# Performance work log

Hardware: AMD Instinct MI355X
Metric: run time of the kernel (lower is better)

Reference implementation:

```python
import jax, jax.numpy as jnp
import numpy as np

N = 50000
E = 800000
IN = 128
H = 128
R = 8
OUT = 2
BN_EPS = 1e-5


def setup_inputs() -> dict:
    key = jax.random.key(0)
    ks = jax.random.split(key, 16)
    s1 = 1.0 / np.sqrt(IN)
    s2 = 1.0 / np.sqrt(H)
    return {
        "x": jax.random.normal(ks[0], (N, IN), dtype=jnp.float32),
        "edge_index": jax.random.randint(ks[1], (2, E), 0, N, dtype=jnp.int32),
        "edge_type": jax.random.randint(ks[2], (E,), 0, R, dtype=jnp.int32),
        # layer 1 RGCNConv params
        "w1": jax.random.normal(ks[3], (R, IN, H), dtype=jnp.float32) * s1,
        "root1": jax.random.normal(ks[4], (IN, H), dtype=jnp.float32) * s1,
        "b1": jnp.zeros((H,), dtype=jnp.float32),
        "g1": jnp.ones((H,), dtype=jnp.float32),
        "be1": jnp.zeros((H,), dtype=jnp.float32),
        # layer 2 RGCNConv params
        "w2": jax.random.normal(ks[5], (R, H, H), dtype=jnp.float32) * s2,
        "root2": jax.random.normal(ks[6], (H, H), dtype=jnp.float32) * s2,
        "b2": jnp.zeros((H,), dtype=jnp.float32),
        "g2": jnp.ones((H,), dtype=jnp.float32),
        "be2": jnp.zeros((H,), dtype=jnp.float32),
        # classifier
        "cw": jax.random.normal(ks[7], (H, OUT), dtype=jnp.float32) * s2,
        "cb": jnp.zeros((OUT,), dtype=jnp.float32),
    }


def rgcn_conv(x, src, tgt, et, W, root, b):
    """PyG-style RGCNConv with per-relation mean aggregation.

    out[v] = sum_r mean_{e: tgt=v, type=r} (x[src_e] @ W[r]) + x[v] @ root + b
    """
    n = x.shape[0]
    # per-(node, relation) in-degree for mean normalization
    comp = tgt * R + et  # composite segment id, [E]
    deg = jax.ops.segment_sum(jnp.ones_like(et, dtype=x.dtype), comp,
                              num_segments=n * R)
    inv_deg = jnp.where(deg > 0, 1.0 / jnp.maximum(deg, 1.0), 0.0)
    # transform every node by every relation weight: [n, R, out]
    xw = jnp.einsum('ni,rio->nro', x, W)
    # gather per-edge message and apply mean normalization: [E, out]
    msg = xw[src, et] * inv_deg[comp][:, None]
    agg = jax.ops.segment_sum(msg, tgt, num_segments=n)
    return agg + x @ root + b


def batchnorm(x, gamma, beta):
    # training-mode BatchNorm1d over node dim (biased variance, eps=1e-5)
    mean = jnp.mean(x, axis=0)
    var = jnp.mean(jnp.square(x - mean), axis=0)
    return gamma * (x - mean) * jax.lax.rsqrt(var + BN_EPS) + beta


def reference(x, edge_index, edge_type, w1, root1, b1, g1, be1,
              w2, root2, b2, g2, be2, cw, cb):
    src, tgt = edge_index[0], edge_index[1]
    h = rgcn_conv(x, src, tgt, edge_type, w1, root1, b1)
    h = jax.nn.relu(batchnorm(h, g1, be1))
    h = rgcn_conv(h, src, tgt, edge_type, w2, root2, b2)
    h = jax.nn.relu(batchnorm(h, g2, be2))
    return h @ cw + cb
```

## Files before the change

kernel.cpp:

```cpp
#include <hip/hip_runtime.h>
#include <hip/hip_bf16.h>

#define N_NODES 50000
#define N_EDGES 800000
#define DIM 128
#define NREL 8
#define KTOT 1152
#define NRSEG (N_NODES * NREL)
#define BN_EPS 1e-5f
#define TILE 32
#define ASTRIDE 136

typedef __attribute__((ext_vector_type(8))) short bf16x8;
typedef __attribute__((ext_vector_type(16))) float f32x16;

__device__ inline float b2f(short s) {
    union { unsigned u; float f; } t;
    t.u = ((unsigned)(unsigned short)s) << 16;
    return t.f;
}
__device__ inline short f2b(float f) {
    __hip_bfloat16 h = __float2bfloat16(f);
    return *reinterpret_cast<short*>(&h);
}


__global__ void k_hist(const int* __restrict__ ei, const int* __restrict__ et,
                       int* __restrict__ cnt) {
    int e = blockIdx.x * 256 + threadIdx.x;
    if (e < N_EDGES) {
        int tgt = ei[N_EDGES + e];
        int r = et[e];
        atomicAdd(&cnt[tgt * NREL + r], 1);
    }
}

__global__ void k_alloc(const int* __restrict__ cnt, int* __restrict__ offs,
                        int* __restrict__ cursor) {
    int i = blockIdx.x * 256 + threadIdx.x;
    int lane = threadIdx.x & 63;
    int c = (i < NRSEG) ? cnt[i] : 0;
    int incl = c;
    #pragma unroll
    for (int d = 1; d < 64; d <<= 1) {
        int t = __shfl_up(incl, d, 64);
        if (lane >= d) incl += t;
    }
    int total = __shfl(incl, 63, 64);
    int base = 0;
    if (lane == 63) base = atomicAdd(cursor, total);
    base = __shfl(base, 63, 64);
    if (i < NRSEG) offs[i] = base + incl - c;
}

__global__ void k_fill(const int* __restrict__ ei, const int* __restrict__ et,
                       const int* __restrict__ offs, int* __restrict__ fillcur,
                       int* __restrict__ sorted) {
    int e = blockIdx.x * 256 + threadIdx.x;
    if (e < N_EDGES) {
        int src = ei[e];
        int tgt = ei[N_EDGES + e];
        int comp = tgt * NREL + et[e];
        int pos = atomicAdd(&fillcur[comp], 1);
        sorted[offs[comp] + pos] = src;
    }
}

__global__ void k_wconv2(const float* __restrict__ W1, const float* __restrict__ root1,
                         __hip_bfloat16* __restrict__ Bt1,
                         const float* __restrict__ W2, const float* __restrict__ root2,
                         __hip_bfloat16* __restrict__ Bt2) {
    int gidx = blockIdx.x * 256 + threadIdx.x;
    int which = gidx >= DIM * KTOT;
    int idx = which ? gidx - DIM * KTOT : gidx;
    const float* W = which ? W2 : W1;
    const float* root = which ? root2 : root1;
    __hip_bfloat16* Bt = which ? Bt2 : Bt1;
    int o = idx / KTOT, k = idx % KTOT;
    float v;
    if (k < NREL * DIM) {
        int r = k >> 7, i = k & 127;
        v = W[(r * DIM + i) * DIM + o];
    } else {
        int i = k - NREL * DIM;
        v = root[i * DIM + o];
    }
    Bt[idx] = __float2bfloat16(v);
}

__global__ void k_cast(const float* __restrict__ in, __hip_bfloat16* __restrict__ out) {
    int i = (blockIdx.x * 256 + threadIdx.x) * 4;
    if (i >= N_NODES * DIM) return;
    float4 v = *(const float4*)&in[i];
    short4 o;
    o.x = f2b(v.x); o.y = f2b(v.y); o.z = f2b(v.z); o.w = f2b(v.w);
    *(short4*)&out[i] = o;
}

__global__ void k_castbn2(const __hip_bfloat16* __restrict__ h, const float* __restrict__ stats,
                          const float* __restrict__ g, const float* __restrict__ be,
                          __hip_bfloat16* __restrict__ xb) {
    int i = (blockIdx.x * 256 + threadIdx.x) * 8;
    if (i >= N_NODES * DIM) return;
    int ch = i & 127;
    bf16x8 v = *(const bf16x8*)&h[i];
    const float invn = 1.f / (float)N_NODES;
    bf16x8 o;
    #pragma unroll
    for (int j = 0; j < 8; ++j) {
        float m = stats[ch + j] * invn;
        float var = stats[128 + ch + j] * invn - m * m;
        float a = g[ch + j] * rsqrtf(var + BN_EPS);
        float b = be[ch + j] - m * a;
        o[j] = f2b(fmaxf(b2f(v[j]) * a + b, 0.f));
    }
    *(bf16x8*)&xb[i] = o;
}

__global__ __launch_bounds__(256) void k_fusedC(
        const __hip_bfloat16* __restrict__ xb,
        const int* __restrict__ cnt, const int* __restrict__ offs,
        const int* __restrict__ sorted,
        const __hip_bfloat16* __restrict__ Bt,
        const float* __restrict__ bias,
        __hip_bfloat16* __restrict__ h, float* __restrict__ stats) {
    __shared__ __hip_bfloat16 At[TILE * ASTRIDE];
    __shared__ int cntS[TILE][NREL];
    __shared__ int offS[TILE][NREL];
    int tid = threadIdx.x;
    int n0 = blockIdx.x * TILE;

    {
        int ni = tid >> 3, r = tid & 7;
        int node = n0 + ni;
        int c = 0, o = 0;
        if (node < N_NODES) {
            c = cnt[node * NREL + r];
            o = offs[node * NREL + r];
        }
        cntS[ni][r] = c;
        offS[ni][r] = o;
    }
    __syncthreads();

    int lane = tid & 63, wid = tid >> 6;
    int half = lane >> 5, l31 = lane & 31;
    const __hip_bfloat16* bBase = Bt + (size_t)(wid * 32 + l31) * KTOT + half * 8;
    f32x16 acc = {};

    int spn = tid >> 4;
    int sub = tid & 15;
    const __hip_bfloat16* xsub = xb + sub * 8;

    #pragma unroll 1
    for (int r = 0; r < 9; ++r) {
        #pragma unroll
        for (int p = 0; p < 2; ++p) {
            int ni = p * 16 + spn;
            if (r < 8) {
                int c = cntS[ni][r];
                int o = offS[ni][r];
                float s[8] = {0.f,0.f,0.f,0.f,0.f,0.f,0.f,0.f};
                for (int i = 0; i < c; ++i) {
                    int idx = sorted[o + i];
                    bf16x8 rv = *(const bf16x8*)(xsub + (size_t)idx * DIM);
                    #pragma unroll
                    for (int j = 0; j < 8; ++j) s[j] += b2f(rv[j]);
                }
                float inv = (c > 0) ? 1.f / (float)c : 0.f;
                bf16x8 ov;
                #pragma unroll
                for (int j = 0; j < 8; ++j) ov[j] = f2b(s[j] * inv);
                *(bf16x8*)&At[ni * ASTRIDE + sub * 8] = ov;
            } else {
                int node = n0 + ni;
                bf16x8 sv = {};
                if (node < N_NODES) sv = *(const bf16x8*)(xsub + (size_t)node * DIM);
                *(bf16x8*)&At[ni * ASTRIDE + sub * 8] = sv;
            }
        }
        __syncthreads();
        const __hip_bfloat16* bs = bBase + r * DIM;
        #pragma unroll
        for (int m = 0; m < 8; ++m) {
            bf16x8 a = *(const bf16x8*)&At[l31 * ASTRIDE + m * 16 + half * 8];
            bf16x8 b = *(const bf16x8*)(bs + m * 16);
            acc = __builtin_amdgcn_mfma_f32_32x32x16_bf16(a, b, acc, 0, 0, 0);
        }
        __syncthreads();
    }

    int col = wid * 32 + l31;
    float bv = bias[col];
    float s1 = 0.f, s2 = 0.f;
    #pragma unroll
    for (int reg = 0; reg < 16; ++reg) {
        int row = n0 + (reg & 3) + 8 * (reg >> 2) + 4 * half;
        float v = acc[reg] + bv;
        if (row < N_NODES) {
            h[(size_t)row * DIM + col] = __float2bfloat16(v);
            s1 += v; s2 += v * v;
        }
    }
    s1 += __shfl_xor(s1, 32, 64);
    s2 += __shfl_xor(s2, 32, 64);
    if (half == 0) {
        atomicAdd(&stats[col], s1);
        atomicAdd(&stats[128 + col], s2);
    }
}

__global__ void k_classifier(const __hip_bfloat16* __restrict__ h, const float* __restrict__ stats,
                             const float* __restrict__ g, const float* __restrict__ be,
                             const float* __restrict__ cw, const float* __restrict__ cb,
                             float* __restrict__ out) {
    int w = blockIdx.x * 4 + (threadIdx.x >> 6);
    int lane = threadIdx.x & 63;
    if (w >= N_NODES) return;
    int c = lane * 2;
    const float invn = 1.f / (float)N_NODES;
    __hip_bfloat162 hv = *(const __hip_bfloat162*)&h[(size_t)w * DIM + c];
    float m0 = stats[c] * invn, var0 = stats[128 + c] * invn - m0 * m0;
    float a0 = g[c] * rsqrtf(var0 + BN_EPS), b0 = be[c] - m0 * a0;
    float m1 = stats[c + 1] * invn, var1 = stats[128 + c + 1] * invn - m1 * m1;
    float a1 = g[c + 1] * rsqrtf(var1 + BN_EPS), b1 = be[c + 1] - m1 * a1;
    float p0 = fmaxf(__bfloat162float(hv.x) * a0 + b0, 0.f);
    float p1 = fmaxf(__bfloat162float(hv.y) * a1 + b1, 0.f);
    float acc0 = p0 * cw[c * 2] + p1 * cw[(c + 1) * 2];
    float acc1 = p0 * cw[c * 2 + 1] + p1 * cw[(c + 1) * 2 + 1];
    #pragma unroll
    for (int d = 32; d; d >>= 1) {
        acc0 += __shfl_down(acc0, d, 64);
        acc1 += __shfl_down(acc1, d, 64);
    }
    if (lane == 0) {
        out[w * 2] = acc0 + cb[0];
        out[w * 2 + 1] = acc1 + cb[1];
    }
}

extern "C" void kernel_launch(void* const* d_in, const int* in_sizes, int n_in,
                              void* d_out, int out_size, void* d_ws, size_t ws_size,
                              hipStream_t stream) {
    const float* x    = (const float*)d_in[0];
    const int*   ei   = (const int*)d_in[1];
    const int*   et   = (const int*)d_in[2];
    const float* w1   = (const float*)d_in[3];
    const float* root1= (const float*)d_in[4];
    const float* b1   = (const float*)d_in[5];
    const float* g1   = (const float*)d_in[6];
    const float* be1  = (const float*)d_in[7];
    const float* w2   = (const float*)d_in[8];
    const float* root2= (const float*)d_in[9];
    const float* b2   = (const float*)d_in[10];
    const float* g2   = (const float*)d_in[11];
    const float* be2  = (const float*)d_in[12];
    const float* cw   = (const float*)d_in[13];
    const float* cb   = (const float*)d_in[14];
    float* out = (float*)d_out;

    char* ws = (char*)d_ws;
    size_t off = 0;
    auto alloc = [&](size_t bytes) -> char* {
        char* p = ws + off;
        off += (bytes + 255) & ~(size_t)255;
        return p;
    };
    int*   cnt     = (int*)alloc((size_t)NRSEG * 4);
    int*   fillcur = (int*)alloc((size_t)NRSEG * 4);
    int*   cursor  = (int*)alloc(256);
    float* stats1  = (float*)alloc(1024);
    float* stats2  = (float*)alloc(1024);
    size_t zero_bytes = off;
    int*   offs    = (int*)alloc((size_t)NRSEG * 4);
    __hip_bfloat16* Bt1 = (__hip_bfloat16*)alloc((size_t)DIM * KTOT * 2);
    __hip_bfloat16* Bt2 = (__hip_bfloat16*)alloc((size_t)DIM * KTOT * 2);
    int*   sorted  = (int*)alloc((size_t)N_EDGES * 4);
    __hip_bfloat16* xb = (__hip_bfloat16*)alloc((size_t)N_NODES * DIM * 2);
    __hip_bfloat16* h1 = (__hip_bfloat16*)alloc((size_t)N_NODES * DIM * 2);
    __hip_bfloat16* h2 = (__hip_bfloat16*)alloc((size_t)N_NODES * DIM * 2);

    hipMemsetAsync(d_ws, 0, zero_bytes, stream);

    k_hist<<<(N_EDGES + 255) / 256, 256, 0, stream>>>(ei, et, cnt);
    k_alloc<<<(NRSEG + 255) / 256, 256, 0, stream>>>(cnt, offs, cursor);
    k_fill<<<(N_EDGES + 255) / 256, 256, 0, stream>>>(ei, et, offs, fillcur, sorted);
    k_wconv2<<<2 * DIM * KTOT / 256, 256, 0, stream>>>(w1, root1, Bt1, w2, root2, Bt2);

    int fgrid = (N_NODES + TILE - 1) / TILE;

    k_cast<<<(N_NODES * DIM / 4 + 255) / 256, 256, 0, stream>>>(x, xb);
    k_fusedC<<<fgrid, 256, 0, stream>>>(xb, cnt, offs, sorted, Bt1, b1, h1, stats1);

    k_castbn2<<<(N_NODES * DIM / 8 + 255) / 256, 256, 0, stream>>>(h1, stats1, g1, be1, xb);
    k_fusedC<<<fgrid, 256, 0, stream>>>(xb, cnt, offs, sorted, Bt2, b2, h2, stats2);

    k_classifier<<<(N_NODES + 3) / 4, 256, 0, stream>>>(h2, stats2, g2, be2, cw, cb, out);
}
```

Baseline: 518.5 us.

## Fuse BN+ReLU into layer-2 gather and interleave two-node unrolled gathers

Removes the separate batchnorm/cast kernel. Layer 2 now reads h1 directly and applies the BN affine transform and ReLU on the fly to every gathered neighbour row and to the root row. The gather loop is also restructured to process two nodes at once, two edges per iteration, with masked loads, so more memory requests are in flight per thread. In exchange, the per-element BN math is recomputed for every edge rather than once per node. The sorted buffer gets padding so the reads past the end of a segment stay in bounds.

```diff
diff --git a/kernel.cpp b/kernel.cpp
--- a/kernel.cpp
+++ b/kernel.cpp
@@ -97,32 +97,15 @@
     *(short4*)&out[i] = o;
 }
 
-__global__ void k_castbn2(const __hip_bfloat16* __restrict__ h, const float* __restrict__ stats,
-                          const float* __restrict__ g, const float* __restrict__ be,
-                          __hip_bfloat16* __restrict__ xb) {
-    int i = (blockIdx.x * 256 + threadIdx.x) * 8;
-    if (i >= N_NODES * DIM) return;
-    int ch = i & 127;
-    bf16x8 v = *(const bf16x8*)&h[i];
-    const float invn = 1.f / (float)N_NODES;
-    bf16x8 o;
-    #pragma unroll
-    for (int j = 0; j < 8; ++j) {
-        float m = stats[ch + j] * invn;
-        float var = stats[128 + ch + j] * invn - m * m;
-        float a = g[ch + j] * rsqrtf(var + BN_EPS);
-        float b = be[ch + j] - m * a;
-        o[j] = f2b(fmaxf(b2f(v[j]) * a + b, 0.f));
-    }
-    *(bf16x8*)&xb[i] = o;
-}
-
-__global__ __launch_bounds__(256) void k_fusedC(
+template<int BN>
+__global__ __launch_bounds__(256) void k_fusedD(
         const __hip_bfloat16* __restrict__ xb,
         const int* __restrict__ cnt, const int* __restrict__ offs,
         const int* __restrict__ sorted,
         const __hip_bfloat16* __restrict__ Bt,
         const float* __restrict__ bias,
+        const float* __restrict__ bnstats, const float* __restrict__ g,
+        const float* __restrict__ be,
         __hip_bfloat16* __restrict__ h, float* __restrict__ stats) {
     __shared__ __hip_bfloat16 At[TILE * ASTRIDE];
     __shared__ int cntS[TILE][NREL];
@@ -141,41 +124,92 @@
         cntS[ni][r] = c;
         offS[ni][r] = o;
     }
-    __syncthreads();
 
     int lane = tid & 63, wid = tid >> 6;
     int half = lane >> 5, l31 = lane & 31;
     const __hip_bfloat16* bBase = Bt + (size_t)(wid * 32 + l31) * KTOT + half * 8;
     f32x16 acc = {};
 
-    int spn = tid >> 4;
-    int sub = tid & 15;
+    int spn = tid >> 4, sub = tid & 15;
     const __hip_bfloat16* xsub = xb + sub * 8;
+
+    float aC[8], bC[8];
+    if (BN) {
+        const float invn = 1.f / (float)N_NODES;
+        #pragma unroll
+        for (int j = 0; j < 8; ++j) {
+            int ch = sub * 8 + j;
+            float m = bnstats[ch] * invn;
+            float var = bnstats[128 + ch] * invn - m * m;
+            float aa = g[ch] * rsqrtf(var + BN_EPS);
+            aC[j] = aa;
+            bC[j] = be[ch] - m * aa;
+        }
+    }
+    __syncthreads();
 
     #pragma unroll 1
     for (int r = 0; r < 9; ++r) {
-        #pragma unroll
-        for (int p = 0; p < 2; ++p) {
-            int ni = p * 16 + spn;
-            if (r < 8) {
-                int c = cntS[ni][r];
-                int o = offS[ni][r];
-                float s[8] = {0.f,0.f,0.f,0.f,0.f,0.f,0.f,0.f};
-                for (int i = 0; i < c; ++i) {
-                    int idx = sorted[o + i];
-                    bf16x8 rv = *(const bf16x8*)(xsub + (size_t)idx * DIM);
-                    #pragma unroll
-                    for (int j = 0; j < 8; ++j) s[j] += b2f(rv[j]);
+        if (r < 8) {
+            int cA = cntS[spn][r],      oA = offS[spn][r];
+            int cB = cntS[spn + 16][r], oB = offS[spn + 16][r];
+            float sA[8] = {0.f,0.f,0.f,0.f,0.f,0.f,0.f,0.f};
+            float sB[8] = {0.f,0.f,0.f,0.f,0.f,0.f,0.f,0.f};
+            int mx = max(cA, cB);
+            #pragma unroll 1
+            for (int i = 0; i < mx; i += 2) {
+                int ja0 = sorted[oA + i];
+                int ja1 = sorted[oA + i + 1];
+                int jb0 = sorted[oB + i];
+                int jb1 = sorted[oB + i + 1];
+                bool vA0 = i < cA, vA1 = i + 1 < cA;
+                bool vB0 = i < cB, vB1 = i + 1 < cB;
+                int ia0 = vA0 ? ja0 : 0;
+                int ia1 = vA1 ? ja1 : 0;
+                int ib0 = vB0 ? jb0 : 0;
+                int ib1 = vB1 ? jb1 : 0;
+                bf16x8 ra0 = *(const bf16x8*)(xsub + (size_t)ia0 * DIM);
+                bf16x8 ra1 = *(const bf16x8*)(xsub + (size_t)ia1 * DIM);
+                bf16x8 rb0 = *(const bf16x8*)(xsub + (size_t)ib0 * DIM);
+                bf16x8 rb1 = *(const bf16x8*)(xsub + (size_t)ib1 * DIM);
+                float ma0 = vA0 ? 1.f : 0.f, ma1 = vA1 ? 1.f : 0.f;
+                float mb0 = vB0 ? 1.f : 0.f, mb1 = vB1 ? 1.f : 0.f;
+                #pragma unroll
+                for (int j = 0; j < 8; ++j) {
+                    float e;
+                    e = b2f(ra0[j]); if (BN) e = fmaxf(fmaf(aC[j], e, bC[j]), 0.f);
+                    sA[j] = fmaf(ma0, e, sA[j]);
+                    e = b2f(ra1[j]); if (BN) e = fmaxf(fmaf(aC[j], e, bC[j]), 0.f);
+                    sA[j] = fmaf(ma1, e, sA[j]);
+                    e = b2f(rb0[j]); if (BN) e = fmaxf(fmaf(aC[j], e, bC[j]), 0.f);
+                    sB[j] = fmaf(mb0, e, sB[j]);
+                    e = b2f(rb1[j]); if (BN) e = fmaxf(fmaf(aC[j], e, bC[j]), 0.f);
+                    sB[j] = fmaf(mb1, e, sB[j]);
                 }
-                float inv = (c > 0) ? 1.f / (float)c : 0.f;
-                bf16x8 ov;
-                #pragma unroll
-                for (int j = 0; j < 8; ++j) ov[j] = f2b(s[j] * inv);
-                *(bf16x8*)&At[ni * ASTRIDE + sub * 8] = ov;
-            } else {
+            }
+            float invA = (cA > 0) ? 1.f / (float)cA : 0.f;
+            float invB = (cB > 0) ? 1.f / (float)cB : 0.f;
+            bf16x8 ovA, ovB;
+            #pragma unroll
+            for (int j = 0; j < 8; ++j) {
+                ovA[j] = f2b(sA[j] * invA);
+                ovB[j] = f2b(sB[j] * invB);
+            }
+            *(bf16x8*)&At[spn * ASTRIDE + sub * 8] = ovA;
+            *(bf16x8*)&At[(spn + 16) * ASTRIDE + sub * 8] = ovB;
+        } else {
+            #pragma unroll
+            for (int p = 0; p < 2; ++p) {
+                int ni = spn + p * 16;
                 int node = n0 + ni;
                 bf16x8 sv = {};
                 if (node < N_NODES) sv = *(const bf16x8*)(xsub + (size_t)node * DIM);
+                if (BN) {
+                    #pragma unroll
+                    for (int j = 0; j < 8; ++j)
+                        sv[j] = f2b(fmaxf(fmaf(aC[j], b2f(sv[j]), bC[j]), 0.f));
+                    if (node >= N_NODES) sv = bf16x8{};
+                }
                 *(bf16x8*)&At[ni * ASTRIDE + sub * 8] = sv;
             }
         }
@@ -275,7 +309,7 @@
     int*   offs    = (int*)alloc((size_t)NRSEG * 4);
     __hip_bfloat16* Bt1 = (__hip_bfloat16*)alloc((size_t)DIM * KTOT * 2);
     __hip_bfloat16* Bt2 = (__hip_bfloat16*)alloc((size_t)DIM * KTOT * 2);
-    int*   sorted  = (int*)alloc((size_t)N_EDGES * 4);
+    int*   sorted  = (int*)alloc((size_t)N_EDGES * 4 + 1024);
     __hip_bfloat16* xb = (__hip_bfloat16*)alloc((size_t)N_NODES * DIM * 2);
     __hip_bfloat16* h1 = (__hip_bfloat16*)alloc((size_t)N_NODES * DIM * 2);
     __hip_bfloat16* h2 = (__hip_bfloat16*)alloc((size_t)N_NODES * DIM * 2);
@@ -290,10 +324,11 @@
     int fgrid = (N_NODES + TILE - 1) / TILE;
 
     k_cast<<<(N_NODES * DIM / 4 + 255) / 256, 256, 0, stream>>>(x, xb);
-    k_fusedC<<<fgrid, 256, 0, stream>>>(xb, cnt, offs, sorted, Bt1, b1, h1, stats1);
-
-    k_castbn2<<<(N_NODES * DIM / 8 + 255) / 256, 256, 0, stream>>>(h1, stats1, g1, be1, xb);
-    k_fusedC<<<fgrid, 256, 0, stream>>>(xb, cnt, offs, sorted, Bt2, b2, h2, stats2);
+    k_fusedD<0><<<fgrid, 256, 0, stream>>>(xb, cnt, offs, sorted, Bt1, b1,
+                                           nullptr, nullptr, nullptr, h1, stats1);
+
+    k_fusedD<1><<<fgrid, 256, 0, stream>>>(h1, cnt, offs, sorted, Bt2, b2,
+                                           stats1, g1, be1, h2, stats2);
 
     k_classifier<<<(N_NODES + 3) / 4, 256, 0, stream>>>(h2, stats2, g2, be2, cw, cb, out);
 }
```

Result: faster. 505.3 us (-2.6%).
